# Optimization experiments

Measured on AMD Instinct MI355X. Metric: run time of the kernel, lower is better.

Reference implementation:

```python
import jax, jax.numpy as jnp
import numpy as np

NUM_GRAPHS = 512

def _add_self_loops(edge_index, n):
    loop = jnp.arange(n, dtype=edge_index.dtype)
    src = jnp.concatenate([edge_index[0], loop])
    dst = jnp.concatenate([edge_index[1], loop])
    return src, dst

def _segment_softmax(e, seg, n):
    m = jax.ops.segment_max(e, seg, num_segments=n)
    e = jnp.exp(e - m[seg])
    s = jax.ops.segment_sum(e, seg, num_segments=n)
    return e / (s[seg] + 1e-16)

def _gat_conv(x, edge_index, W, a_src, a_dst, b, heads, ch):
    n = x.shape[0]
    src, dst = _add_self_loops(edge_index, n)
    h = (x @ W).reshape(n, heads, ch)                      # [N,H,C]
    al = (h * a_src).sum(-1)                               # [N,H]
    ar = (h * a_dst).sum(-1)                               # [N,H]
    e = jax.nn.leaky_relu(al[src] + ar[dst], 0.2)          # [E,H]
    alpha = _segment_softmax(e, dst, n)                    # [E,H]
    out = jax.ops.segment_sum(h[src] * alpha[:, :, None], dst, num_segments=n)
    return out.reshape(n, heads * ch) + b

def _gcn_conv(x, edge_index, W, b):
    n = x.shape[0]
    src, dst = _add_self_loops(edge_index, n)
    h = x @ W
    deg = jax.ops.segment_sum(jnp.ones(dst.shape, h.dtype), dst, num_segments=n)
    dis = jax.lax.rsqrt(jnp.maximum(deg, 1.0))
    norm = dis[src] * dis[dst]
    return jax.ops.segment_sum(h[src] * norm[:, None], dst, num_segments=n) + b

def _gmp(x, batch):
    return jax.ops.segment_max(x, batch, num_segments=NUM_GRAPHS)

def setup_inputs() -> dict:
    key = jax.random.key(0)
    ks = jax.random.split(key, 24)
    nd, ed = 100000, 800000
    np_, ep = 300000, 2400000
    def rn(k, shape, scale=0.1):
        return jax.random.normal(k, shape, dtype=jnp.float32) * scale
    inp = {
        "x_drug": jax.random.normal(ks[0], (nd, 78), dtype=jnp.float32),
        "edge_index_drug": jax.random.randint(ks[1], (2, ed), 0, nd, dtype=jnp.int32),
        "batch_drug": jnp.sort(jax.random.randint(ks[2], (nd,), 0, NUM_GRAPHS, dtype=jnp.int32)),
        "x_prot": jax.random.normal(ks[3], (np_, 41), dtype=jnp.float32),
        "edge_index_prot": jax.random.randint(ks[4], (2, ep), 0, np_, dtype=jnp.int32),
        "batch_prot": jnp.sort(jax.random.randint(ks[5], (np_,), 0, NUM_GRAPHS, dtype=jnp.int32)),
        # GATConv1: 78 -> 78, heads=10
        "W1": rn(ks[6], (78, 780)), "a_src1": rn(ks[7], (10, 78)), "a_dst1": rn(ks[8], (10, 78)), "b1": jnp.zeros((780,), jnp.float32),
        # GATConv2: 780 -> 128, heads=1
        "W2": rn(ks[9], (780, 128), 0.05), "a_src2": rn(ks[10], (1, 128)), "a_dst2": rn(ks[11], (1, 128)), "b2": jnp.zeros((128,), jnp.float32),
        "fc_g1_W": rn(ks[12], (128, 128)), "fc_g1_b": jnp.zeros((128,), jnp.float32),
        "gcn1_W": rn(ks[13], (41, 41)), "gcn1_b": jnp.zeros((41,), jnp.float32),
        "gcn2_W": rn(ks[14], (41, 64)), "gcn2_b": jnp.zeros((64,), jnp.float32),
        "lin1_W": rn(ks[15], (64, 128)), "lin1_b": jnp.zeros((128,), jnp.float32),
        "fc1_W": rn(ks[16], (256, 1024), 0.05), "fc1_b": jnp.zeros((1024,), jnp.float32),
        "fc2_W": rn(ks[17], (1024, 256), 0.03), "fc2_b": jnp.zeros((256,), jnp.float32),
        "out_W": rn(ks[18], (256, 1)), "out_b": jnp.zeros((1,), jnp.float32),
    }
    return inp

def reference(x_drug, edge_index_drug, batch_drug, x_prot, edge_index_prot, batch_prot,
              W1, a_src1, a_dst1, b1, W2, a_src2, a_dst2, b2, fc_g1_W, fc_g1_b,
              gcn1_W, gcn1_b, gcn2_W, gcn2_b, lin1_W, lin1_b,
              fc1_W, fc1_b, fc2_W, fc2_b, out_W, out_b):
    # drug branch (eval mode: dropout = identity)
    xd = jax.nn.elu(_gat_conv(x_drug, edge_index_drug, W1, a_src1, a_dst1, b1, 10, 78))
    xd = jax.nn.relu(_gat_conv(xd, edge_index_drug, W2, a_src2, a_dst2, b2, 1, 128))
    xd = _gmp(xd, batch_drug)
    xd = jax.nn.relu(xd @ fc_g1_W + fc_g1_b)
    # protein branch
    xp = jax.nn.relu(_gcn_conv(x_prot, edge_index_prot, gcn1_W, gcn1_b))
    xp = jax.nn.relu(_gcn_conv(xp, edge_index_prot, gcn2_W, gcn2_b))
    xp = _gmp(xp, batch_prot)
    xp = jax.nn.relu(xp @ lin1_W + lin1_b)
    # head
    xc = jnp.concatenate([xd, xp], axis=1)
    xc = jax.nn.relu(xc @ fc1_W + fc1_b)
    xc = jax.nn.relu(xc @ fc2_W + fc2_b)
    return xc @ out_W + out_b
```

## Files before the change

kernel.cpp:

```cpp
#include <hip/hip_runtime.h>
#include <math.h>

static inline int cdiv(int a, int b) { return (a + b - 1) / b; }

typedef __attribute__((ext_vector_type(8))) short short8v;
typedef __attribute__((ext_vector_type(4))) float f32x4;

__device__ inline unsigned bf16rne(float x) {
  unsigned u = __builtin_bit_cast(unsigned, x);
  return (u + 0x7FFFu + ((u >> 16) & 1u)) >> 16;
}
__device__ inline float bfhi(unsigned h) { return __builtin_bit_cast(float, h << 16); }
__device__ inline unsigned pk(float v) {
  unsigned hb = bf16rne(v);
  return hb | (bf16rne(v - bfhi(hb)) << 16);
}

__global__ void k_count(const int* __restrict__ dst, int E, int* __restrict__ cnt) {
  int i = blockIdx.x * 256 + threadIdx.x;
  if (i < E) atomicAdd(&cnt[dst[i]], 1);
}

__global__ __launch_bounds__(256) void k_scan_chunk(const int* __restrict__ in, int n,
                                                    int* __restrict__ out, int* __restrict__ sums) {
  __shared__ int tsum[256];
  int base = blockIdx.x * 1024;
  int t = threadIdx.x;
  int v[4]; int s = 0;
#pragma unroll
  for (int i = 0; i < 4; i++) { int idx = base + t * 4 + i; int x = (idx < n) ? in[idx] : 0; v[i] = x; s += x; }
  tsum[t] = s;
  __syncthreads();
  int x = s;
  for (int off = 1; off < 256; off <<= 1) {
    int y = (t >= off) ? tsum[t - off] : 0;
    __syncthreads();
    x += y;
    tsum[t] = x;
    __syncthreads();
  }
  int run = x - s;
#pragma unroll
  for (int i = 0; i < 4; i++) { int idx = base + t * 4 + i; if (idx < n) out[idx] = run; run += v[i]; }
  if (t == 255 && sums) sums[blockIdx.x] = x;
}

__global__ void k_scan_add(int* __restrict__ out, int n, const int* __restrict__ se,
                           int total, int* __restrict__ cur) {
  int i = blockIdx.x * 256 + threadIdx.x;
  if (i < n) { int v = out[i] + se[i >> 10]; out[i] = v; cur[i] = v; }
  if (i == 0) out[n] = total;
}

__global__ void k_fillr(const int* __restrict__ src, const int* __restrict__ dst, int E,
                        int* __restrict__ cur, int* __restrict__ adj, int lo, int hi) {
  int i = blockIdx.x * 256 + threadIdx.x;
  if (i < E) {
    int d = dst[i];
    if (d >= lo && d < hi) { int p = atomicAdd(&cur[d], 1); adj[p] = src[i]; }
  }
}

__global__ void k_w1t_pk(const float* __restrict__ W1, unsigned* __restrict__ o) {
  int i = blockIdx.x * 256 + threadIdx.x;
  if (i < 60840) { int h = i / 6084, r = i % 6084, c = r / 78, k = r % 78;
    o[i] = pk(W1[(size_t)k * 780 + h * 78 + c]); }
}
__global__ void k_w2t_pk(const float* __restrict__ W2, unsigned* __restrict__ o) {
  int i = blockIdx.x * 256 + threadIdx.x;
  if (i < 99840) { int n = i / 780, k = i % 780;
    o[i] = pk(W2[(size_t)k * 128 + n]); }
}

__global__ void k_vsrc(const float* __restrict__ W1, const float* __restrict__ a_src,
                       const float* __restrict__ a_dst, float* __restrict__ Vs, float* __restrict__ Vd) {
  int t = blockIdx.x * 64 + threadIdx.x;
  if (t >= 780) return;
  int k = t / 10, h = t % 10;
  float ss = 0.f, sd = 0.f;
  for (int c = 0; c < 78; c++) {
    float w = W1[k * 780 + h * 78 + c];
    ss += w * a_src[h * 78 + c];
    sd += w * a_dst[h * 78 + c];
  }
  Vs[k * 10 + h] = ss; Vd[k * 10 + h] = sd;
}

__global__ void k_alar1(const float* __restrict__ x, const float* __restrict__ Vs,
                        const float* __restrict__ Vd, float* __restrict__ al,
                        float* __restrict__ ar, int nd) {
  int t = blockIdx.x * 256 + threadIdx.x;
  if (t >= nd * 10) return;
  int n = t / 10, h = t % 10;
  const float* xr = x + (size_t)n * 78;
  float sa = 0.f, sd = 0.f;
  for (int k = 0; k < 78; k++) { float xv = xr[k]; sa += xv * Vs[k * 10 + h]; sd += xv * Vd[k * 10 + h]; }
  al[t] = sa; ar[t] = sd;
}

__global__ __launch_bounds__(64) void k_gat_agg1(const float* __restrict__ x, const int* __restrict__ adj,
                                                 const int* __restrict__ roff, const float* __restrict__ al,
                                                 const float* __restrict__ ar, unsigned* __restrict__ zp, int node0) {
  int n = node0 + blockIdx.x;
  int lane = threadIdx.x;
  int rs = roff[n];
  int deg = roff[n + 1] - rs;
  int tot = deg + 1;
  __shared__ float m_s[10], is_s[10], ar_s[10];
  __shared__ float red_s[64];
  __shared__ int src_s[64];
  __shared__ float alpha_s[64][10];
  if (lane < 10) ar_s[lane] = ar[n * 10 + lane];
  __syncthreads();
  int h = lane % 10; int eL = lane / 10;
  float mx = -1e30f;
  if (lane < 60) {
    for (int e = eL; e < tot; e += 6) {
      int s = (e == deg) ? n : adj[rs + e];
      float v = al[s * 10 + h] + ar_s[h];
      v = (v >= 0.f) ? v : 0.2f * v;
      mx = fmaxf(mx, v);
    }
  }
  red_s[lane] = mx;
  __syncthreads();
  if (lane < 10) {
    float m = red_s[lane];
    for (int g = 1; g < 6; g++) m = fmaxf(m, red_s[lane + g * 10]);
    m_s[lane] = m;
  }
  __syncthreads();
  float sm = 0.f;
  if (lane < 60) {
    float m = m_s[h];
    for (int e = eL; e < tot; e += 6) {
      int s = (e == deg) ? n : adj[rs + e];
      float v = al[s * 10 + h] + ar_s[h];
      v = (v >= 0.f) ? v : 0.2f * v;
      sm += __expf(v - m);
    }
  }
  red_s[lane] = sm;
  __syncthreads();
  if (lane < 10) {
    float s = 0.f;
    for (int g = 0; g < 6; g++) s += red_s[lane + g * 10];
    is_s[lane] = 1.f / (s + 1e-16f);
  }
  __syncthreads();
  float zA[10], zB[10];
#pragma unroll
  for (int i = 0; i < 10; i++) { zA[i] = 0.f; zB[i] = 0.f; }
  for (int c0 = 0; c0 < tot; c0 += 64) {
    int csz = (tot - c0 < 64) ? (tot - c0) : 64;
    if (lane < csz) {
      int e = c0 + lane;
      src_s[lane] = (e == deg) ? n : adj[rs + e];
    }
    __syncthreads();
    for (int p = lane; p < csz * 10; p += 64) {
      int e = p / 10; int hh = p % 10;
      int s = src_s[e];
      float v = al[s * 10 + hh] + ar_s[hh];
      v = (v >= 0.f) ? v : 0.2f * v;
      alpha_s[e][hh] = __expf(v - m_s[hh]) * is_s[hh];
    }
    __syncthreads();
    for (int e = 0; e < csz; e++) {
      int s = src_s[e];
      float xa = x[(size_t)s * 78 + lane];
      float xb = (lane < 14) ? x[(size_t)s * 78 + 64 + lane] : 0.f;
#pragma unroll
      for (int hh = 0; hh < 10; hh++) {
        float a = alpha_s[e][hh];
        zA[hh] += a * xa;
        zB[hh] += a * xb;
      }
    }
    __syncthreads();
  }
  unsigned* zr = zp + (size_t)blockIdx.x * 780;
#pragma unroll
  for (int hh = 0; hh < 10; hh++) {
    zr[hh * 78 + lane] = pk(zA[hh]);
    if (lane < 14) zr[hh * 78 + 64 + lane] = pk(zB[hh]);
  }
}

template <int RT, int CT, int MODE>
__global__ __launch_bounds__(256) void k_mfpk(const unsigned* __restrict__ Ap, const unsigned* __restrict__ Btp,
                                              const float* __restrict__ bias, float* __restrict__ C,
                                              unsigned* __restrict__ Op,
                                              int M, int N, int K, int lda, int ldb, int ldc,
                                              int hsA, int hsB, int hsBias) {
  const int BM = RT * 32, BN = CT * 32;
  __shared__ short Ah[BM][40], Al[BM][40], Bh[BN][40], Bl[BN][40];
  size_t aoff = (size_t)blockIdx.y * hsA;
  size_t boff = (size_t)blockIdx.y * hsB;
  if (bias) bias += (size_t)blockIdx.y * hsBias;
  int t = threadIdx.x;
  int bm = blockIdx.x * BM;
  int bn = blockIdx.z * BN;
  int w = t >> 6, l = t & 63;
  int wy = w >> 1, wx = w & 1;
  int lm = l & 15, lk = (l >> 4) * 8;

  f32x4 acc[RT][CT];
#pragma unroll
  for (int i = 0; i < RT; i++)
#pragma unroll
    for (int j = 0; j < CT; j++) acc[i][j] = (f32x4){0.f, 0.f, 0.f, 0.f};

  for (int k0 = 0; k0 < K; k0 += 32) {
    for (int i = t; i < BM * 16; i += 256) {
      int m = i >> 4, kp = (i & 15) * 2;
      int gm = bm + m, gk = k0 + kp;
      unsigned w0 = 0, w1 = 0;
      if (gm < M) {
        if (gk < K) w0 = Ap[aoff + (size_t)gm * lda + gk];
        if (gk + 1 < K) w1 = Ap[aoff + (size_t)gm * lda + gk + 1];
      }
      *(unsigned*)&Ah[m][kp] = (w0 & 0xFFFFu) | (w1 << 16);
      *(unsigned*)&Al[m][kp] = (w0 >> 16) | (w1 & 0xFFFF0000u);
    }
    for (int i = t; i < BN * 16; i += 256) {
      int n = i >> 4, kp = (i & 15) * 2;
      int gn = bn + n, gk = k0 + kp;
      unsigned w0 = 0, w1 = 0;
      if (gn < N) {
        if (gk < K) w0 = Btp[boff + (size_t)gn * ldb + gk];
        if (gk + 1 < K) w1 = Btp[boff + (size_t)gn * ldb + gk + 1];
      }
      *(unsigned*)&Bh[n][kp] = (w0 & 0xFFFFu) | (w1 << 16);
      *(unsigned*)&Bl[n][kp] = (w0 >> 16) | (w1 & 0xFFFF0000u);
    }
    __syncthreads();
    short8v bhf[CT], blf[CT];
#pragma unroll
    for (int ct = 0; ct < CT; ct++) {
      int col = wx * (CT * 16) + ct * 16 + lm;
      bhf[ct] = *(const short8v*)&Bh[col][lk];
      blf[ct] = *(const short8v*)&Bl[col][lk];
    }
#pragma unroll
    for (int rt = 0; rt < RT; rt++) {
      int row = wy * (RT * 16) + rt * 16 + lm;
      short8v ah = *(const short8v*)&Ah[row][lk];
      short8v alo = *(const short8v*)&Al[row][lk];
#pragma unroll
      for (int ct = 0; ct < CT; ct++) {
        acc[rt][ct] = __builtin_amdgcn_mfma_f32_16x16x32_bf16(ah, bhf[ct], acc[rt][ct], 0, 0, 0);
        acc[rt][ct] = __builtin_amdgcn_mfma_f32_16x16x32_bf16(ah, blf[ct], acc[rt][ct], 0, 0, 0);
        acc[rt][ct] = __builtin_amdgcn_mfma_f32_16x16x32_bf16(alo, bhf[ct], acc[rt][ct], 0, 0, 0);
      }
    }
    __syncthreads();
  }
#pragma unroll
  for (int rt = 0; rt < RT; rt++) {
#pragma unroll
    for (int r = 0; r < 4; r++) {
      int gm = bm + wy * (RT * 16) + rt * 16 + (l >> 4) * 4 + r;
      if (gm >= M) continue;
#pragma unroll
      for (int ct = 0; ct < CT; ct++) {
        int gn = bn + wx * (CT * 16) + ct * 16 + lm;
        if (gn >= N) continue;
        float v = acc[rt][ct][r] + (bias ? bias[gn] : 0.f);
        if (MODE == 0) {
          C[(size_t)gm * ldc + gn] = v;
        } else {
          v = (v > 0.f) ? v : (__expf(v) - 1.f);
          Op[aoff + (size_t)gm * lda + gn] = pk(v);
        }
      }
    }
  }
}

template <int ACT>
__global__ __launch_bounds__(256) void k_gemm(const float* __restrict__ A, const float* __restrict__ B,
                                              const float* __restrict__ bias, float* __restrict__ C,
                                              int M, int N, int K, int lda, int ldb, int ldc) {
  __shared__ float As[16][68];
  __shared__ float Bs[16][68];
  int tx = threadIdx.x % 16, ty = threadIdx.x / 16;
  int bm = blockIdx.x * 64, bn = blockIdx.y * 64;
  float acc[4][4] = {};
  for (int k0 = 0; k0 < K; k0 += 16) {
    for (int i = threadIdx.x; i < 1024; i += 256) {
      int r = i / 16, kk = i % 16;
      int gm = bm + r, gk = k0 + kk;
      As[kk][r] = (gm < M && gk < K) ? A[(size_t)gm * lda + gk] : 0.f;
    }
    for (int i = threadIdx.x; i < 1024; i += 256) {
      int kk = i / 64, c = i % 64;
      int gk = k0 + kk, gn = bn + c;
      Bs[kk][c] = (gk < K && gn < N) ? B[(size_t)gk * ldb + gn] : 0.f;
    }
    __syncthreads();
#pragma unroll
    for (int kk = 0; kk < 16; kk++) {
      float a[4], b[4];
#pragma unroll
      for (int i = 0; i < 4; i++) a[i] = As[kk][ty * 4 + i];
#pragma unroll
      for (int j = 0; j < 4; j++) b[j] = Bs[kk][tx * 4 + j];
#pragma unroll
      for (int i = 0; i < 4; i++)
#pragma unroll
        for (int j = 0; j < 4; j++) acc[i][j] += a[i] * b[j];
    }
    __syncthreads();
  }
#pragma unroll
  for (int i = 0; i < 4; i++) {
    int gm = bm + ty * 4 + i;
    if (gm >= M) continue;
#pragma unroll
    for (int j = 0; j < 4; j++) {
      int gn = bn + tx * 4 + j;
      if (gn >= N) continue;
      float v = acc[i][j] + (bias ? bias[gn] : 0.f);
      if (ACT == 1) v = fmaxf(v, 0.f);
      else if (ACT == 2) v = (v > 0.f) ? v : (__expf(v) - 1.f);
      C[(size_t)gm * ldc + gn] = v;
    }
  }
}

__global__ __launch_bounds__(64) void k_alar2(const float* __restrict__ h2, const float* __restrict__ a_src,
                                              const float* __restrict__ a_dst, float* __restrict__ al,
                                              float* __restrict__ ar) {
  int n = blockIdx.x, lane = threadIdx.x;
  float v0 = h2[(size_t)n * 128 + lane], v1 = h2[(size_t)n * 128 + 64 + lane];
  float sa = v0 * a_src[lane] + v1 * a_src[64 + lane];
  float sd = v0 * a_dst[lane] + v1 * a_dst[64 + lane];
#pragma unroll
  for (int o = 32; o; o >>= 1) { sa += __shfl_xor(sa, o); sd += __shfl_xor(sd, o); }
  if (lane == 0) { al[n] = sa; ar[n] = sd; }
}

__global__ __launch_bounds__(64) void k_gat_agg2(const float* __restrict__ h2, const int* __restrict__ adj,
                                                 const int* __restrict__ roff, const float* __restrict__ al,
                                                 const float* __restrict__ ar, const float* __restrict__ b2,
                                                 float* __restrict__ out) {
  int n = blockIdx.x, lane = threadIdx.x;
  int rs = roff[n];
  int deg = roff[n + 1] - rs;
  int tot = deg + 1;
  float arn = ar[n];
  float mx = -1e30f;
  for (int e = lane; e < tot; e += 64) {
    int s = (e == deg) ? n : adj[rs + e];
    float v = al[s] + arn; v = (v >= 0.f) ? v : 0.2f * v;
    mx = fmaxf(mx, v);
  }
#pragma unroll
  for (int o = 32; o; o >>= 1) mx = fmaxf(mx, __shfl_xor(mx, o));
  float sm = 0.f;
  for (int e = lane; e < tot; e += 64) {
    int s = (e == deg) ? n : adj[rs + e];
    float v = al[s] + arn; v = (v >= 0.f) ? v : 0.2f * v;
    sm += __expf(v - mx);
  }
#pragma unroll
  for (int o = 32; o; o >>= 1) sm += __shfl_xor(sm, o);
  float inv = 1.f / (sm + 1e-16f);
  float a0 = 0.f, a1 = 0.f;
  for (int e = 0; e < tot; e++) {
    int s = (e == deg) ? n : adj[rs + e];
    float v = al[s] + arn; v = (v >= 0.f) ? v : 0.2f * v;
    float alpha = __expf(v - mx) * inv;
    a0 += alpha * h2[(size_t)s * 128 + lane];
    a1 += alpha * h2[(size_t)s * 128 + 64 + lane];
  }
  out[(size_t)n * 128 + lane]      = fmaxf(a0 + b2[lane], 0.f);
  out[(size_t)n * 128 + 64 + lane] = fmaxf(a1 + b2[64 + lane], 0.f);
}

__global__ void k_dis(const int* __restrict__ roff, float* __restrict__ dis, int n) {
  int i = blockIdx.x * 256 + threadIdx.x;
  if (i < n) dis[i] = rsqrtf((float)(roff[i + 1] - roff[i] + 1));
}

__global__ __launch_bounds__(64) void k_gcn_agg(const float* __restrict__ h, const int* __restrict__ adj,
                                                const int* __restrict__ roff, const float* __restrict__ dis,
                                                const float* __restrict__ bias, float* __restrict__ out, int C) {
  int n = blockIdx.x, lane = threadIdx.x;
  int rs = roff[n], re = roff[n + 1];
  float dn = dis[n];
  bool act = lane < C;
  float acc = 0.f;
  for (int e = rs; e < re; e++) {
    int s = adj[e];
    float w = dis[s];
    if (act) acc += w * h[(size_t)s * C + lane];
  }
  if (act) {
    acc += dn * h[(size_t)n * C + lane];
    float v = dn * acc + bias[lane];
    out[(size_t)n * C + lane] = fmaxf(v, 0.f);
  }
}

__global__ void k_bounds(const int* __restrict__ batch, int n, int* __restrict__ gstart, int G) {
  int i = blockIdx.x * 256 + threadIdx.x;
  if (i >= n) return;
  int b = batch[i];
  if (i == 0) { for (int g = 0; g <= b; g++) gstart[g] = 0; }
  else { int p = batch[i - 1]; for (int g = p + 1; g <= b; g++) gstart[g] = i; }
  if (i == n - 1) { for (int g = b + 1; g <= G; g++) gstart[g] = n; }
}

__global__ __launch_bounds__(256) void k_pool(const float* __restrict__ xin, const int* __restrict__ gstart,
                                              float* __restrict__ pool, int C) {
  int g = blockIdx.x; int t = threadIdx.x;
  int groups = 256 / C;
  int grp = t / C, c = t % C;
  __shared__ float red[256];
  int n0 = gstart[g], n1 = gstart[g + 1];
  float m = -3.4e38f;
  for (int i = n0 + grp; i < n1; i += groups) m = fmaxf(m, xin[(size_t)i * C + c]);
  red[t] = m;
  __syncthreads();
  if (grp == 0) {
    for (int q = 1; q < groups; q++) m = fmaxf(m, red[q * C + c]);
    pool[(size_t)g * C + c] = m;
  }
}

__global__ __launch_bounds__(256) void k_head(const float* __restrict__ pd, const float* __restrict__ pp,
                                              const float* __restrict__ fcgW, const float* __restrict__ fcgb,
                                              const float* __restrict__ l1W, const float* __restrict__ l1b,
                                              const float* __restrict__ f1W, const float* __restrict__ f1b,
                                              const float* __restrict__ f2W, const float* __restrict__ f2b,
                                              const float* __restrict__ oW, const float* __restrict__ ob,
                                              float* __restrict__ out) {
  int g = blockIdx.x, t = threadIdx.x;
  __shared__ float pds[128], pps[64], xcs[256], t1s[1024];
  __shared__ float red[4];
  if (t < 128) pds[t] = pd[(size_t)g * 128 + t];
  else if (t < 192) pps[t - 128] = pp[(size_t)g * 64 + (t - 128)];
  __syncthreads();
  float a = 0.f;
  if (t < 128) {
#pragma unroll 8
    for (int k = 0; k < 128; k++) a += pds[k] * fcgW[k * 128 + t];
    a = fmaxf(a + fcgb[t], 0.f);
  } else {
    int c = t - 128;
#pragma unroll 8
    for (int k = 0; k < 64; k++) a += pps[k] * l1W[k * 128 + c];
    a = fmaxf(a + l1b[c], 0.f);
  }
  xcs[t] = a;
  __syncthreads();
  float acc0 = 0.f, acc1 = 0.f, acc2 = 0.f, acc3 = 0.f;
#pragma unroll 4
  for (int k = 0; k < 256; k++) {
    float xv = xcs[k];
    const float* rw = f1W + (size_t)k * 1024 + t;
    acc0 += xv * rw[0];
    acc1 += xv * rw[256];
    acc2 += xv * rw[512];
    acc3 += xv * rw[768];
  }
  t1s[t]       = fmaxf(acc0 + f1b[t], 0.f);
  t1s[t + 256] = fmaxf(acc1 + f1b[t + 256], 0.f);
  t1s[t + 512] = fmaxf(acc2 + f1b[t + 512], 0.f);
  t1s[t + 768] = fmaxf(acc3 + f1b[t + 768], 0.f);
  __syncthreads();
  float v = 0.f;
#pragma unroll 8
  for (int k = 0; k < 1024; k++) v += t1s[k] * f2W[k * 256 + t];
  v = fmaxf(v + f2b[t], 0.f);
  float s = v * oW[t];
#pragma unroll
  for (int o = 32; o; o >>= 1) s += __shfl_xor(s, o);
  if ((t & 63) == 0) red[t >> 6] = s;
  __syncthreads();
  if (t == 0) out[g] = red[0] + red[1] + red[2] + red[3] + ob[0];
}

extern "C" void kernel_launch(void* const* d_in, const int* in_sizes, int n_in,
                              void* d_out, int out_size, void* d_ws, size_t ws_size,
                              hipStream_t stream) {
  if (n_in < 28) return;
  const float* x_drug  = (const float*)d_in[0];
  const int*   ei_d    = (const int*)d_in[1];
  const int*   batch_d = (const int*)d_in[2];
  const float* x_prot  = (const float*)d_in[3];
  const int*   ei_p    = (const int*)d_in[4];
  const int*   batch_p = (const int*)d_in[5];
  const float* W1     = (const float*)d_in[6];
  const float* a_src1 = (const float*)d_in[7];
  const float* a_dst1 = (const float*)d_in[8];
  const float* b1     = (const float*)d_in[9];
  const float* W2     = (const float*)d_in[10];
  const float* a_src2 = (const float*)d_in[11];
  const float* a_dst2 = (const float*)d_in[12];
  const float* b2     = (const float*)d_in[13];
  const float* fcgW = (const float*)d_in[14];
  const float* fcgb = (const float*)d_in[15];
  const float* g1W  = (const float*)d_in[16];
  const float* g1b  = (const float*)d_in[17];
  const float* g2W  = (const float*)d_in[18];
  const float* g2b  = (const float*)d_in[19];
  const float* l1W  = (const float*)d_in[20];
  const float* l1b  = (const float*)d_in[21];
  const float* f1W  = (const float*)d_in[22];
  const float* f1b  = (const float*)d_in[23];
  const float* f2W  = (const float*)d_in[24];
  const float* f2b  = (const float*)d_in[25];
  const float* oW   = (const float*)d_in[26];
  const float* ob   = (const float*)d_in[27];

  const int nd = in_sizes[0] / 78, ed = in_sizes[1] / 2;
  const int np = in_sizes[3] / 41, ep = in_sizes[4] / 2;
  const int G = 512;

  char* Bp = (char*)d_ws;
  size_t cap = ws_size;
  auto atop = [&](size_t bytes) -> char* {
    cap = (cap - bytes) & ~(size_t)255;
    return Bp + cap;
  };
  float* pooled_d = (float*)atop((size_t)G * 128 * 4);
  float* pooled_p = (float*)atop((size_t)G * 64 * 4);
  int* gs_d = (int*)atop(513 * 4);
  int* gs_p = (int*)atop(513 * 4);
  unsigned* W1tp = (unsigned*)atop(60840 * 4);
  unsigned* W2tp = (unsigned*)atop(99840 * 4);

  size_t off = 0;
  auto alc = [&](size_t bytes) -> char* {
    char* p = Bp + off;
    off = (off + bytes + 255) & ~(size_t)255;
    return p;
  };

  k_w1t_pk<<<cdiv(60840, 256), 256, 0, stream>>>(W1, W1tp);
  k_w2t_pk<<<cdiv(99840, 256), 256, 0, stream>>>(W2, W2tp);

  int* cur_d  = (int*)alc((size_t)nd * 4);
  int* roff_d = (int*)alc(((size_t)nd + 1) * 4);
  int* adj_d  = (int*)alc((size_t)ed * 4);
  int* part   = (int*)alc(1024 * 4);
  int* parte  = (int*)alc(1024 * 4);
  float* Vs  = (float*)alc(780 * 4);
  float* Vd  = (float*)alc(780 * 4);
  float* al1 = (float*)alc((size_t)nd * 10 * 4);
  float* ar1 = (float*)alc((size_t)nd * 10 * 4);
  float* al2 = (float*)alc((size_t)nd * 4);
  float* ar2 = (float*)alc((size_t)nd * 4);
  float* h2  = (float*)alc((size_t)nd * 128 * 4);

  size_t remain = (cap > off) ? cap - off : 0;
  size_t xd2_bytes = (size_t)nd * 128 * 4;
  unsigned* zp; float* xd2;
  long long slabCap;
  if (remain >= xd2_bytes + (size_t)128 * 3120) {
    xd2 = (float*)(Bp + off);
    slabCap = (long long)(remain / 3120);
  } else {
    xd2 = (float*)alc(xd2_bytes);
    size_t r2 = (cap > off) ? cap - off : 0;
    slabCap = (long long)(r2 / 3120);
  }
  int slabN = (int)((slabCap < (long long)nd) ? slabCap : (long long)nd);
  slabN &= ~127;
  if (slabN < 128) slabN = 128;
  zp = (unsigned*)(Bp + off);

  hipMemsetAsync(cur_d, 0, (size_t)nd * 4, stream);
  k_count<<<cdiv(ed, 256), 256, 0, stream>>>(ei_d + ed, ed, cur_d);
  int nch = cdiv(nd, 1024);
  k_scan_chunk<<<nch, 256, 0, stream>>>(cur_d, nd, roff_d, part);
  k_scan_chunk<<<1, 256, 0, stream>>>(part, nch, parte, nullptr);
  k_scan_add<<<cdiv(nd, 256), 256, 0, stream>>>(roff_d, nd, parte, ed, cur_d);
  {
    const int NP = 4;
    for (int p = 0; p < NP; p++) {
      int lo = (int)((long long)nd * p / NP);
      int hi = (int)((long long)nd * (p + 1) / NP);
      k_fillr<<<cdiv(ed, 256), 256, 0, stream>>>(ei_d, ei_d + ed, ed, cur_d, adj_d, lo, hi);
    }
  }

  k_vsrc<<<cdiv(780, 64), 64, 0, stream>>>(W1, a_src1, a_dst1, Vs, Vd);
  k_alar1<<<cdiv(nd * 10, 256), 256, 0, stream>>>(x_drug, Vs, Vd, al1, ar1, nd);

  for (int s0 = 0; s0 < nd; s0 += slabN) {
    int sm = ((nd - s0) < slabN) ? (nd - s0) : slabN;
    k_gat_agg1<<<sm, 64, 0, stream>>>(x_drug, adj_d, roff_d, al1, ar1, zp, s0);
    k_mfpk<2, 3, 2><<<dim3(cdiv(sm, 64), 10, 1), 256, 0, stream>>>(
        zp, W1tp, b1, nullptr, zp, sm, 78, 78, 780, 78, 0, 78, 6084, 78);
    k_mfpk<2, 4, 0><<<dim3(cdiv(sm, 64), 1, 1), 256, 0, stream>>>(
        zp, W2tp, nullptr, h2 + (size_t)s0 * 128, nullptr,
        sm, 128, 780, 780, 780, 128, 0, 0, 0);
  }
  k_alar2<<<nd, 64, 0, stream>>>(h2, a_src2, a_dst2, al2, ar2);
  k_gat_agg2<<<nd, 64, 0, stream>>>(h2, adj_d, roff_d, al2, ar2, b2, xd2);
  k_bounds<<<cdiv(nd, 256), 256, 0, stream>>>(batch_d, nd, gs_d, G);
  k_pool<<<G, 256, 0, stream>>>(xd2, gs_d, pooled_d, 128);

  off = 0;
  int* cur_p  = (int*)alc((size_t)np * 4);
  int* roff_p = (int*)alc(((size_t)np + 1) * 4);
  int* adj_p  = (int*)alc((size_t)ep * 4);
  int* partp  = (int*)alc(1024 * 4);
  int* partep = (int*)alc(1024 * 4);
  float* dis = (float*)alc((size_t)np * 4);
  float* hp1 = (float*)alc((size_t)np * 41 * 4);
  float* xp1 = (float*)alc((size_t)np * 41 * 4);
  float* hp2 = (float*)alc((size_t)np * 64 * 4);
  float* xp2 = hp1;

  hipMemsetAsync(cur_p, 0, (size_t)np * 4, stream);
  k_count<<<cdiv(ep, 256), 256, 0, stream>>>(ei_p + ep, ep, cur_p);
  int nchp = cdiv(np, 1024);
  k_scan_chunk<<<nchp, 256, 0, stream>>>(cur_p, np, roff_p, partp);
  k_scan_chunk<<<1, 256, 0, stream>>>(partp, nchp, partep, nullptr);
  k_scan_add<<<cdiv(np, 256), 256, 0, stream>>>(roff_p, np, partep, ep, cur_p);
  {
    const int NP = 10;
    for (int p = 0; p < NP; p++) {
      int lo = (int)((long long)np * p / NP);
      int hi = (int)((long long)np * (p + 1) / NP);
      k_fillr<<<cdiv(ep, 256), 256, 0, stream>>>(ei_p, ei_p + ep, ep, cur_p, adj_p, lo, hi);
    }
  }
  k_dis<<<cdiv(np, 256), 256, 0, stream>>>(roff_p, dis, np);

  k_gemm<0><<<dim3(cdiv(np, 64), 1), 256, 0, stream>>>(x_prot, g1W, nullptr, hp1, np, 41, 41, 41, 41, 41);
  k_gcn_agg<<<np, 64, 0, stream>>>(hp1, adj_p, roff_p, dis, g1b, xp1, 41);
  k_gemm<0><<<dim3(cdiv(np, 64), 1), 256, 0, stream>>>(xp1, g2W, nullptr, hp2, np, 64, 41, 41, 64, 64);
  k_gcn_agg<<<np, 64, 0, stream>>>(hp2, adj_p, roff_p, dis, g2b, xp2, 64);
  k_bounds<<<cdiv(np, 256), 256, 0, stream>>>(batch_p, np, gs_p, G);
  k_pool<<<G, 256, 0, stream>>>(xp2, gs_p, pooled_p, 64);

  k_head<<<G, 256, 0, stream>>>(pooled_d, pooled_p, fcgW, fcgb, l1W, l1b,
                                f1W, f1b, f2W, f2b, oW, ob, (float*)d_out);
}
```

Baseline: 1.866 ms.

## Fuse per-head GAT1 projection with ELU into the W2 GEMM in shared memory

Replaces the two k_mfpk launches (a per-head 78x78 GEMM with bias+ELU writing packed results back to zp, then a 780->128 GEMM reading zp) with a single kernel. Each block computes one head's 64x78 tile, applies bias and ELU into shared memory as hi/lo bf16, and immediately accumulates it against the matching W2 slice. This removes the global write and re-read of the 780-wide intermediate and one launch per slab. In exchange each block now handles all 10 heads serially, giving ten times fewer blocks per slab, uses more shared memory and keeps both accumulator sets live, which may cut occupancy.

```diff
diff --git a/kernel.cpp b/kernel.cpp
--- a/kernel.cpp
+++ b/kernel.cpp
@@ -187,95 +187,145 @@
   }
 }
 
-template <int RT, int CT, int MODE>
-__global__ __launch_bounds__(256) void k_mfpk(const unsigned* __restrict__ Ap, const unsigned* __restrict__ Btp,
-                                              const float* __restrict__ bias, float* __restrict__ C,
-                                              unsigned* __restrict__ Op,
-                                              int M, int N, int K, int lda, int ldb, int ldc,
-                                              int hsA, int hsB, int hsBias) {
-  const int BM = RT * 32, BN = CT * 32;
-  __shared__ short Ah[BM][40], Al[BM][40], Bh[BN][40], Bl[BN][40];
-  size_t aoff = (size_t)blockIdx.y * hsA;
-  size_t boff = (size_t)blockIdx.y * hsB;
-  if (bias) bias += (size_t)blockIdx.y * hsBias;
+__global__ __launch_bounds__(256) void k_fuse(const unsigned* __restrict__ zp, const unsigned* __restrict__ W1tp,
+                                              const float* __restrict__ b1, const unsigned* __restrict__ W2tp,
+                                              float* __restrict__ h2o, int M) {
+  __shared__ short Ah[64][40], Al[64][40];
+  __shared__ short Bh[128][40], Bl[128][40];
+  __shared__ short Xh[64][96], Xl[64][96];
   int t = threadIdx.x;
-  int bm = blockIdx.x * BM;
-  int bn = blockIdx.z * BN;
+  int bm = blockIdx.x * 64;
   int w = t >> 6, l = t & 63;
   int wy = w >> 1, wx = w & 1;
   int lm = l & 15, lk = (l >> 4) * 8;
 
-  f32x4 acc[RT][CT];
-#pragma unroll
-  for (int i = 0; i < RT; i++)
-#pragma unroll
-    for (int j = 0; j < CT; j++) acc[i][j] = (f32x4){0.f, 0.f, 0.f, 0.f};
-
-  for (int k0 = 0; k0 < K; k0 += 32) {
-    for (int i = t; i < BM * 16; i += 256) {
-      int m = i >> 4, kp = (i & 15) * 2;
-      int gm = bm + m, gk = k0 + kp;
-      unsigned w0 = 0, w1 = 0;
-      if (gm < M) {
-        if (gk < K) w0 = Ap[aoff + (size_t)gm * lda + gk];
-        if (gk + 1 < K) w1 = Ap[aoff + (size_t)gm * lda + gk + 1];
-      }
-      *(unsigned*)&Ah[m][kp] = (w0 & 0xFFFFu) | (w1 << 16);
-      *(unsigned*)&Al[m][kp] = (w0 >> 16) | (w1 & 0xFFFF0000u);
-    }
-    for (int i = t; i < BN * 16; i += 256) {
-      int n = i >> 4, kp = (i & 15) * 2;
-      int gn = bn + n, gk = k0 + kp;
-      unsigned w0 = 0, w1 = 0;
-      if (gn < N) {
-        if (gk < K) w0 = Btp[boff + (size_t)gn * ldb + gk];
-        if (gk + 1 < K) w1 = Btp[boff + (size_t)gn * ldb + gk + 1];
-      }
-      *(unsigned*)&Bh[n][kp] = (w0 & 0xFFFFu) | (w1 << 16);
-      *(unsigned*)&Bl[n][kp] = (w0 >> 16) | (w1 & 0xFFFF0000u);
-    }
-    __syncthreads();
-    short8v bhf[CT], blf[CT];
-#pragma unroll
-    for (int ct = 0; ct < CT; ct++) {
-      int col = wx * (CT * 16) + ct * 16 + lm;
-      bhf[ct] = *(const short8v*)&Bh[col][lk];
-      blf[ct] = *(const short8v*)&Bl[col][lk];
-    }
-#pragma unroll
-    for (int rt = 0; rt < RT; rt++) {
-      int row = wy * (RT * 16) + rt * 16 + lm;
-      short8v ah = *(const short8v*)&Ah[row][lk];
-      short8v alo = *(const short8v*)&Al[row][lk];
-#pragma unroll
-      for (int ct = 0; ct < CT; ct++) {
-        acc[rt][ct] = __builtin_amdgcn_mfma_f32_16x16x32_bf16(ah, bhf[ct], acc[rt][ct], 0, 0, 0);
-        acc[rt][ct] = __builtin_amdgcn_mfma_f32_16x16x32_bf16(ah, blf[ct], acc[rt][ct], 0, 0, 0);
-        acc[rt][ct] = __builtin_amdgcn_mfma_f32_16x16x32_bf16(alo, bhf[ct], acc[rt][ct], 0, 0, 0);
-      }
-    }
-    __syncthreads();
-  }
-#pragma unroll
-  for (int rt = 0; rt < RT; rt++) {
+  for (int i = t; i < 64 * 18; i += 256) {
+    int r = i / 18, c = 78 + i % 18;
+    Xh[r][c] = 0; Xl[r][c] = 0;
+  }
+
+  f32x4 acc2[2][4];
+#pragma unroll
+  for (int i = 0; i < 2; i++)
+#pragma unroll
+    for (int j = 0; j < 4; j++) acc2[i][j] = (f32x4){0.f, 0.f, 0.f, 0.f};
+
+  for (int h = 0; h < 10; h++) {
+    const unsigned* W1h = W1tp + h * 6084;
+    f32x4 acc1[2][3];
+#pragma unroll
+    for (int i = 0; i < 2; i++)
+#pragma unroll
+      for (int j = 0; j < 3; j++) acc1[i][j] = (f32x4){0.f, 0.f, 0.f, 0.f};
+
+    for (int k0 = 0; k0 < 78; k0 += 32) {
+      for (int i = t; i < 64 * 16; i += 256) {
+        int m = i >> 4, kp = (i & 15) * 2;
+        int gm = bm + m, gk = k0 + kp;
+        unsigned w0 = 0, w1 = 0;
+        if (gm < M) {
+          if (gk < 78) w0 = zp[(size_t)gm * 780 + h * 78 + gk];
+          if (gk + 1 < 78) w1 = zp[(size_t)gm * 780 + h * 78 + gk + 1];
+        }
+        *(unsigned*)&Ah[m][kp] = (w0 & 0xFFFFu) | (w1 << 16);
+        *(unsigned*)&Al[m][kp] = (w0 >> 16) | (w1 & 0xFFFF0000u);
+      }
+      for (int i = t; i < 96 * 16; i += 256) {
+        int n = i >> 4, kp = (i & 15) * 2;
+        int gk = k0 + kp;
+        unsigned w0 = 0, w1 = 0;
+        if (n < 78) {
+          if (gk < 78) w0 = W1h[(size_t)n * 78 + gk];
+          if (gk + 1 < 78) w1 = W1h[(size_t)n * 78 + gk + 1];
+        }
+        *(unsigned*)&Bh[n][kp] = (w0 & 0xFFFFu) | (w1 << 16);
+        *(unsigned*)&Bl[n][kp] = (w0 >> 16) | (w1 & 0xFFFF0000u);
+      }
+      __syncthreads();
+      short8v bh[3], bl[3];
+#pragma unroll
+      for (int ct = 0; ct < 3; ct++) {
+        int col = wx * 48 + ct * 16 + lm;
+        bh[ct] = *(const short8v*)&Bh[col][lk];
+        bl[ct] = *(const short8v*)&Bl[col][lk];
+      }
+#pragma unroll
+      for (int rt = 0; rt < 2; rt++) {
+        int row = wy * 32 + rt * 16 + lm;
+        short8v ah = *(const short8v*)&Ah[row][lk];
+        short8v alo = *(const short8v*)&Al[row][lk];
+#pragma unroll
+        for (int ct = 0; ct < 3; ct++) {
+          acc1[rt][ct] = __builtin_amdgcn_mfma_f32_16x16x32_bf16(ah, bh[ct], acc1[rt][ct], 0, 0, 0);
+          acc1[rt][ct] = __builtin_amdgcn_mfma_f32_16x16x32_bf16(ah, bl[ct], acc1[rt][ct], 0, 0, 0);
+          acc1[rt][ct] = __builtin_amdgcn_mfma_f32_16x16x32_bf16(alo, bh[ct], acc1[rt][ct], 0, 0, 0);
+        }
+      }
+      __syncthreads();
+    }
+#pragma unroll
+    for (int rt = 0; rt < 2; rt++)
+#pragma unroll
+      for (int r = 0; r < 4; r++) {
+        int row = wy * 32 + rt * 16 + (l >> 4) * 4 + r;
+#pragma unroll
+        for (int ct = 0; ct < 3; ct++) {
+          int col = wx * 48 + ct * 16 + lm;
+          if (col < 78) {
+            float v = acc1[rt][ct][r] + b1[h * 78 + col];
+            v = (v > 0.f) ? v : (__expf(v) - 1.f);
+            unsigned hb = bf16rne(v);
+            Xh[row][col] = (short)hb;
+            Xl[row][col] = (short)bf16rne(v - bfhi(hb));
+          }
+        }
+      }
+    __syncthreads();
+    for (int k0 = 0; k0 < 78; k0 += 32) {
+      for (int i = t; i < 128 * 16; i += 256) {
+        int n = i >> 4, kp = (i & 15) * 2;
+        int gk = k0 + kp;
+        unsigned w0 = 0, w1 = 0;
+        if (gk < 78) w0 = W2tp[(size_t)n * 780 + h * 78 + gk];
+        if (gk + 1 < 78) w1 = W2tp[(size_t)n * 780 + h * 78 + gk + 1];
+        *(unsigned*)&Bh[n][kp] = (w0 & 0xFFFFu) | (w1 << 16);
+        *(unsigned*)&Bl[n][kp] = (w0 >> 16) | (w1 & 0xFFFF0000u);
+      }
+      __syncthreads();
+      short8v bh[4], bl[4];
+#pragma unroll
+      for (int ct = 0; ct < 4; ct++) {
+        int col = wx * 64 + ct * 16 + lm;
+        bh[ct] = *(const short8v*)&Bh[col][lk];
+        bl[ct] = *(const short8v*)&Bl[col][lk];
+      }
+#pragma unroll
+      for (int rt = 0; rt < 2; rt++) {
+        int row = wy * 32 + rt * 16 + lm;
+        short8v ah = *(const short8v*)&Xh[row][k0 + lk];
+        short8v alo = *(const short8v*)&Xl[row][k0 + lk];
+#pragma unroll
+        for (int ct = 0; ct < 4; ct++) {
+          acc2[rt][ct] = __builtin_amdgcn_mfma_f32_16x16x32_bf16(ah, bh[ct], acc2[rt][ct], 0, 0, 0);
+          acc2[rt][ct] = __builtin_amdgcn_mfma_f32_16x16x32_bf16(ah, bl[ct], acc2[rt][ct], 0, 0, 0);
+          acc2[rt][ct] = __builtin_amdgcn_mfma_f32_16x16x32_bf16(alo, bh[ct], acc2[rt][ct], 0, 0, 0);
+        }
+      }
+      __syncthreads();
+    }
+  }
+#pragma unroll
+  for (int rt = 0; rt < 2; rt++)
 #pragma unroll
     for (int r = 0; r < 4; r++) {
-      int gm = bm + wy * (RT * 16) + rt * 16 + (l >> 4) * 4 + r;
+      int gm = bm + wy * 32 + rt * 16 + (l >> 4) * 4 + r;
       if (gm >= M) continue;
 #pragma unroll
-      for (int ct = 0; ct < CT; ct++) {
-        int gn = bn + wx * (CT * 16) + ct * 16 + lm;
-        if (gn >= N) continue;
-        float v = acc[rt][ct][r] + (bias ? bias[gn] : 0.f);
-        if (MODE == 0) {
-          C[(size_t)gm * ldc + gn] = v;
-        } else {
-          v = (v > 0.f) ? v : (__expf(v) - 1.f);
-          Op[aoff + (size_t)gm * lda + gn] = pk(v);
-        }
-      }
-    }
-  }
+      for (int ct = 0; ct < 4; ct++) {
+        int gn = wx * 64 + ct * 16 + lm;
+        h2o[(size_t)gm * 128 + gn] = acc2[rt][ct][r];
+      }
+    }
 }
 
 template <int ACT>
@@ -594,11 +644,7 @@
   for (int s0 = 0; s0 < nd; s0 += slabN) {
     int sm = ((nd - s0) < slabN) ? (nd - s0) : slabN;
     k_gat_agg1<<<sm, 64, 0, stream>>>(x_drug, adj_d, roff_d, al1, ar1, zp, s0);
-    k_mfpk<2, 3, 2><<<dim3(cdiv(sm, 64), 10, 1), 256, 0, stream>>>(
-        zp, W1tp, b1, nullptr, zp, sm, 78, 78, 780, 78, 0, 78, 6084, 78);
-    k_mfpk<2, 4, 0><<<dim3(cdiv(sm, 64), 1, 1), 256, 0, stream>>>(
-        zp, W2tp, nullptr, h2 + (size_t)s0 * 128, nullptr,
-        sm, 128, 780, 780, 780, 128, 0, 0, 0);
+    k_fuse<<<cdiv(sm, 64), 256, 0, stream>>>(zp, W1tp, b1, W2tp, h2 + (size_t)s0 * 128, sm);
   }
   k_alar2<<<nd, 64, 0, stream>>>(h2, a_src2, a_dst2, al2, ar2);
   k_gat_agg2<<<nd, 64, 0, stream>>>(h2, adj_d, roff_d, al2, ar2, b2, xd2);
```

Result: slower. 2.112 ms (+13.2%).
